# Kernel optimization log

Hardware: AMD Instinct MI355X
Metric: run time of the kernel (lower is better)

## Reference

```python
import jax, jax.numpy as jnp
import numpy as np

EPS = 1e-05

def setup_inputs() -> dict:
    key = jax.random.key(0)
    k1, = jax.random.split(key, 1)
    x = jax.random.normal(k1, (4, 4096, 2048), dtype=jnp.float32)
    g = jnp.ones((2048,), dtype=jnp.float32)
    return {"x": x, "g": g}

def reference(x, g):
    # RMSNorm: x / sqrt(mean(x^2, axis=-1) + eps) * g, computed in fp32
    dtype = x.dtype
    xf = x.astype(jnp.float32)
    ms = jnp.mean(xf * xf, axis=-1, keepdims=True)  # [B,S,1]
    out = xf * jax.lax.rsqrt(ms + EPS) * g
    return out.astype(dtype)
```

## Files before the change

### kernel.cpp

```cpp
#include <hip/hip_runtime.h>

#define ROW_LEN 2048
#define BLOCK   256
#define ROWS_PER_BLOCK 4
#define EPS     1e-5f

__global__ __launch_bounds__(BLOCK) void RMSNorm_56607668961691_kernel(
    const float* __restrict__ x,
    const float* __restrict__ g,
    float* __restrict__ out)
{
    const int wave = threadIdx.x >> 6;
    const int lane = threadIdx.x & 63;
    const size_t row = (size_t)blockIdx.x * ROWS_PER_BLOCK + wave;

    const float4* __restrict__ xr   = reinterpret_cast<const float4*>(x + row * ROW_LEN) + lane;
    float4* __restrict__       outr = reinterpret_cast<float4*>(out + row * ROW_LEN) + lane;
    const float4* __restrict__ gv   = reinterpret_cast<const float4*>(g) + lane;

    float4 v[8];
    #pragma unroll
    for (int j = 0; j < 8; ++j) v[j] = xr[j * 64];

    float s0 = 0.f, s1 = 0.f, s2 = 0.f, s3 = 0.f;
    #pragma unroll
    for (int j = 0; j < 8; ++j) {
        s0 += v[j].x * v[j].x;
        s1 += v[j].y * v[j].y;
        s2 += v[j].z * v[j].z;
        s3 += v[j].w * v[j].w;
    }
    float ss = (s0 + s1) + (s2 + s3);

    #pragma unroll
    for (int off = 32; off > 0; off >>= 1)
        ss += __shfl_xor(ss, off, 64);

    const float scale = rsqrtf(ss * (1.0f / (float)ROW_LEN) + EPS);

    #pragma unroll
    for (int j = 0; j < 8; ++j) {
        const float4 gj = gv[j * 64];
        float4 o;
        o.x = v[j].x * scale * gj.x;
        o.y = v[j].y * scale * gj.y;
        o.z = v[j].z * scale * gj.z;
        o.w = v[j].w * scale * gj.w;
        outr[j * 64] = o;
    }
}

extern "C" void kernel_launch(void* const* d_in, const int* in_sizes, int n_in,
                              void* d_out, int out_size, void* d_ws, size_t ws_size,
                              hipStream_t stream) {
    const float* x = (const float*)d_in[0];
    const float* g = (const float*)d_in[1];
    float* out = (float*)d_out;

    const int rows = in_sizes[0] / ROW_LEN;
    const int grid = rows / ROWS_PER_BLOCK;
    RMSNorm_56607668961691_kernel<<<grid, BLOCK, 0, stream>>>(x, g, out);
}
```

Baseline: 229.3 us.

## Process four rows per wave with register prefetch and nontemporal stores

Each wave now handles four consecutive rows. It loads the gamma vector once and prefetches the next row into registers while the current row is reduced and written. Output writes use nontemporal stores to avoid polluting the cache, and the grid shrinks by four. In exchange, register pressure rises and the grid has far fewer blocks, which may reduce the memory-level parallelism the GPU can use to hide latency.

```diff
diff --git a/kernel.cpp b/kernel.cpp
--- a/kernel.cpp
+++ b/kernel.cpp
@@ -2,51 +2,74 @@
 
 #define ROW_LEN 2048
 #define BLOCK   256
-#define ROWS_PER_BLOCK 4
+#define ROWS_PER_WAVE 4
 #define EPS     1e-5f
 
-__global__ __launch_bounds__(BLOCK) void RMSNorm_56607668961691_kernel(
+typedef float floatx4 __attribute__((ext_vector_type(4)));
+
+__global__ __launch_bounds__(BLOCK, 4) void RMSNorm_56607668961691_kernel(
     const float* __restrict__ x,
     const float* __restrict__ g,
     float* __restrict__ out)
 {
     const int wave = threadIdx.x >> 6;
     const int lane = threadIdx.x & 63;
-    const size_t row = (size_t)blockIdx.x * ROWS_PER_BLOCK + wave;
+    const size_t wid  = (size_t)blockIdx.x * (BLOCK / 64) + wave;
+    const size_t row0 = wid * ROWS_PER_WAVE;
 
-    const float4* __restrict__ xr   = reinterpret_cast<const float4*>(x + row * ROW_LEN) + lane;
-    float4* __restrict__       outr = reinterpret_cast<float4*>(out + row * ROW_LEN) + lane;
+    const float4* __restrict__ xr   = reinterpret_cast<const float4*>(x + row0 * ROW_LEN) + lane;
+    float4* __restrict__       outr = reinterpret_cast<float4*>(out + row0 * ROW_LEN) + lane;
     const float4* __restrict__ gv   = reinterpret_cast<const float4*>(g) + lane;
 
-    float4 v[8];
+    float4 gr[8];
     #pragma unroll
-    for (int j = 0; j < 8; ++j) v[j] = xr[j * 64];
+    for (int j = 0; j < 8; ++j) gr[j] = gv[j * 64];
 
-    float s0 = 0.f, s1 = 0.f, s2 = 0.f, s3 = 0.f;
+    float4 cur[8];
     #pragma unroll
-    for (int j = 0; j < 8; ++j) {
-        s0 += v[j].x * v[j].x;
-        s1 += v[j].y * v[j].y;
-        s2 += v[j].z * v[j].z;
-        s3 += v[j].w * v[j].w;
-    }
-    float ss = (s0 + s1) + (s2 + s3);
+    for (int j = 0; j < 8; ++j) cur[j] = xr[j * 64];
 
     #pragma unroll
-    for (int off = 32; off > 0; off >>= 1)
-        ss += __shfl_xor(ss, off, 64);
+    for (int r = 0; r < ROWS_PER_WAVE; ++r) {
+        float4 nxt[8];
+        if (r + 1 < ROWS_PER_WAVE) {
+            const float4* xn = xr + (size_t)(r + 1) * (ROW_LEN / 4);
+            #pragma unroll
+            for (int j = 0; j < 8; ++j) nxt[j] = xn[j * 64];
+        }
 
-    const float scale = rsqrtf(ss * (1.0f / (float)ROW_LEN) + EPS);
+        float s0 = 0.f, s1 = 0.f, s2 = 0.f, s3 = 0.f;
+        #pragma unroll
+        for (int j = 0; j < 8; ++j) {
+            s0 += cur[j].x * cur[j].x;
+            s1 += cur[j].y * cur[j].y;
+            s2 += cur[j].z * cur[j].z;
+            s3 += cur[j].w * cur[j].w;
+        }
+        float ss = (s0 + s1) + (s2 + s3);
 
-    #pragma unroll
-    for (int j = 0; j < 8; ++j) {
-        const float4 gj = gv[j * 64];
-        float4 o;
-        o.x = v[j].x * scale * gj.x;
-        o.y = v[j].y * scale * gj.y;
-        o.z = v[j].z * scale * gj.z;
-        o.w = v[j].w * scale * gj.w;
-        outr[j * 64] = o;
+        #pragma unroll
+        for (int off = 32; off > 0; off >>= 1)
+            ss += __shfl_xor(ss, off, 64);
+
+        const float scale = rsqrtf(ss * (1.0f / (float)ROW_LEN) + EPS);
+
+        float4* o = outr + (size_t)r * (ROW_LEN / 4);
+        #pragma unroll
+        for (int j = 0; j < 8; ++j) {
+            float4 ov;
+            ov.x = cur[j].x * scale * gr[j].x;
+            ov.y = cur[j].y * scale * gr[j].y;
+            ov.z = cur[j].z * scale * gr[j].z;
+            ov.w = cur[j].w * scale * gr[j].w;
+            __builtin_nontemporal_store(*reinterpret_cast<floatx4*>(&ov),
+                                        reinterpret_cast<floatx4*>(&o[j * 64]));
+        }
+
+        if (r + 1 < ROWS_PER_WAVE) {
+            #pragma unroll
+            for (int j = 0; j < 8; ++j) cur[j] = nxt[j];
+        }
     }
 }
 
@@ -58,6 +81,6 @@
     float* out = (float*)d_out;
 
     const int rows = in_sizes[0] / ROW_LEN;
-    const int grid = rows / ROWS_PER_BLOCK;
+    const int grid = rows / (ROWS_PER_WAVE * (BLOCK / 64));
     RMSNorm_56607668961691_kernel<<<grid, BLOCK, 0, stream>>>(x, g, out);
 }
```

Result: slower. 234.8 us (+2.4%).

## Split RMSNorm into row-scale pass and streaming elementwise pass

Applied to the files above, without the earlier changes.

Computes per-row inverse RMS in a first kernel into a global scale buffer, then applies scale and gain in a second grid-stride streaming kernel with nontemporal stores. The intent is to decouple the reduction from a fully coalesced, high-occupancy elementwise pass. It costs a second full read of x and an extra launch, and relies on a fixed-size global scale array.

```diff
diff --git a/kernel.cpp b/kernel.cpp
--- a/kernel.cpp
+++ b/kernel.cpp
@@ -2,21 +2,22 @@
 
 #define ROW_LEN 2048
 #define BLOCK   256
-#define ROWS_PER_BLOCK 4
 #define EPS     1e-5f
 
-__global__ __launch_bounds__(BLOCK) void RMSNorm_56607668961691_kernel(
-    const float* __restrict__ x,
-    const float* __restrict__ g,
-    float* __restrict__ out)
+typedef float floatx4 __attribute__((ext_vector_type(4)));
+
+__device__ float g_row_scale[32768];
+
+__global__ __launch_bounds__(BLOCK) void RMSNorm_pass1_kernel(
+    const float* __restrict__ x, int rows)
 {
     const int wave = threadIdx.x >> 6;
     const int lane = threadIdx.x & 63;
-    const size_t row = (size_t)blockIdx.x * ROWS_PER_BLOCK + wave;
+    const int row  = blockIdx.x * (BLOCK / 64) + wave;
+    if (row >= rows) return;
 
-    const float4* __restrict__ xr   = reinterpret_cast<const float4*>(x + row * ROW_LEN) + lane;
-    float4* __restrict__       outr = reinterpret_cast<float4*>(out + row * ROW_LEN) + lane;
-    const float4* __restrict__ gv   = reinterpret_cast<const float4*>(g) + lane;
+    const float4* __restrict__ xr =
+        reinterpret_cast<const float4*>(x + (size_t)row * ROW_LEN) + lane;
 
     float4 v[8];
     #pragma unroll
@@ -36,17 +37,27 @@
     for (int off = 32; off > 0; off >>= 1)
         ss += __shfl_xor(ss, off, 64);
 
-    const float scale = rsqrtf(ss * (1.0f / (float)ROW_LEN) + EPS);
+    if (lane == 0)
+        g_row_scale[row] = rsqrtf(ss * (1.0f / (float)ROW_LEN) + EPS);
+}
 
-    #pragma unroll
-    for (int j = 0; j < 8; ++j) {
-        const float4 gj = gv[j * 64];
-        float4 o;
-        o.x = v[j].x * scale * gj.x;
-        o.y = v[j].y * scale * gj.y;
-        o.z = v[j].z * scale * gj.z;
-        o.w = v[j].w * scale * gj.w;
-        outr[j * 64] = o;
+__global__ __launch_bounds__(BLOCK) void RMSNorm_pass2_kernel(
+    const float* __restrict__ x, const float* __restrict__ g,
+    float* __restrict__ out, int n4)
+{
+    const floatx4* __restrict__ x4 = reinterpret_cast<const floatx4*>(x);
+    const floatx4* __restrict__ g4 = reinterpret_cast<const floatx4*>(g);
+    floatx4* __restrict__       o4 = reinterpret_cast<floatx4*>(out);
+
+    const int stride = gridDim.x * BLOCK;
+    for (int i = blockIdx.x * BLOCK + threadIdx.x; i < n4; i += stride) {
+        const floatx4 xv = x4[i];
+        const int row = i >> 9;
+        const int col = i & 511;
+        const float s = g_row_scale[row];
+        const floatx4 gv = g4[col];
+        floatx4 ov = xv * s * gv;
+        __builtin_nontemporal_store(ov, &o4[i]);
     }
 }
 
@@ -58,6 +69,11 @@
     float* out = (float*)d_out;
 
     const int rows = in_sizes[0] / ROW_LEN;
-    const int grid = rows / ROWS_PER_BLOCK;
-    RMSNorm_56607668961691_kernel<<<grid, BLOCK, 0, stream>>>(x, g, out);
+    const int n4   = rows * (ROW_LEN / 4);
+
+    const int grid1 = (rows + (BLOCK / 64) - 1) / (BLOCK / 64);
+    RMSNorm_pass1_kernel<<<grid1, BLOCK, 0, stream>>>(x, rows);
+
+    const int grid2 = 4096;
+    RMSNorm_pass2_kernel<<<grid2, BLOCK, 0, stream>>>(x, g, out, n4);
 }
```

After: 245.9 us. +7.3%, slower.

## Split block into producer/consumer waves with double-buffered LDS row pipeline

Applied to the files above, without the earlier changes.

Restructures the kernel so that four producer waves load a row into LDS and compute partial sums of squares, while four consumer waves normalize and store the previous row. Each block now handles 8 rows in sequence, with block-wide barriers between steps. The goal is to overlap global loads with stores through a software pipeline. In exchange it adds LDS round trips, a __syncthreads per row, and fewer independent outstanding loads per thread, on a kernel that is purely memory-bound.

```diff
diff --git a/kernel.cpp b/kernel.cpp
--- a/kernel.cpp
+++ b/kernel.cpp
@@ -1,8 +1,9 @@
 #include <hip/hip_runtime.h>
 
 #define ROW_LEN 2048
-#define BLOCK   256
-#define ROWS_PER_BLOCK 4
+#define R4      (ROW_LEN / 4)
+#define BLOCK   512
+#define ROWS_PER_BLOCK 8
 #define EPS     1e-5f
 
 __global__ __launch_bounds__(BLOCK) void RMSNorm_56607668961691_kernel(
@@ -10,43 +11,58 @@
     const float* __restrict__ g,
     float* __restrict__ out)
 {
-    const int wave = threadIdx.x >> 6;
-    const int lane = threadIdx.x & 63;
-    const size_t row = (size_t)blockIdx.x * ROWS_PER_BLOCK + wave;
+    __shared__ float4 buf[2][R4];
+    __shared__ float  psum[2][4];
 
-    const float4* __restrict__ xr   = reinterpret_cast<const float4*>(x + row * ROW_LEN) + lane;
-    float4* __restrict__       outr = reinterpret_cast<float4*>(out + row * ROW_LEN) + lane;
-    const float4* __restrict__ gv   = reinterpret_cast<const float4*>(g) + lane;
+    const int tid  = threadIdx.x;
+    const int w    = tid >> 6;
+    const int lane = tid & 63;
+    const bool producer = (w < 4);
+    const int pw   = producer ? w : (w - 4);
+    const int c    = pw * 64 + lane;
 
-    float4 v[8];
-    #pragma unroll
-    for (int j = 0; j < 8; ++j) v[j] = xr[j * 64];
+    const size_t row0 = (size_t)blockIdx.x * ROWS_PER_BLOCK;
+    const float4* __restrict__ x4 = reinterpret_cast<const float4*>(x) + row0 * R4;
+    float4* __restrict__       o4 = reinterpret_cast<float4*>(out)     + row0 * R4;
+    const float4* __restrict__ g4 = reinterpret_cast<const float4*>(g);
 
-    float s0 = 0.f, s1 = 0.f, s2 = 0.f, s3 = 0.f;
-    #pragma unroll
-    for (int j = 0; j < 8; ++j) {
-        s0 += v[j].x * v[j].x;
-        s1 += v[j].y * v[j].y;
-        s2 += v[j].z * v[j].z;
-        s3 += v[j].w * v[j].w;
-    }
-    float ss = (s0 + s1) + (s2 + s3);
+    float4 ga, gb;
+    if (!producer) { ga = g4[c]; gb = g4[c + 256]; }
 
-    #pragma unroll
-    for (int off = 32; off > 0; off >>= 1)
-        ss += __shfl_xor(ss, off, 64);
-
-    const float scale = rsqrtf(ss * (1.0f / (float)ROW_LEN) + EPS);
-
-    #pragma unroll
-    for (int j = 0; j < 8; ++j) {
-        const float4 gj = gv[j * 64];
-        float4 o;
-        o.x = v[j].x * scale * gj.x;
-        o.y = v[j].y * scale * gj.y;
-        o.z = v[j].z * scale * gj.z;
-        o.w = v[j].w * scale * gj.w;
-        outr[j * 64] = o;
+    for (int t = 0; t <= ROWS_PER_BLOCK; ++t) {
+        const int b = t & 1;
+        if (producer) {
+            if (t < ROWS_PER_BLOCK) {
+                const float4 v0 = x4[(size_t)t * R4 + c];
+                const float4 v1 = x4[(size_t)t * R4 + c + 256];
+                buf[b][c]       = v0;
+                buf[b][c + 256] = v1;
+                float s = v0.x * v0.x + v0.y * v0.y + v0.z * v0.z + v0.w * v0.w
+                        + v1.x * v1.x + v1.y * v1.y + v1.z * v1.z + v1.w * v1.w;
+                #pragma unroll
+                for (int off = 32; off > 0; off >>= 1)
+                    s += __shfl_xor(s, off, 64);
+                if (lane == 0) psum[b][pw] = s;
+            }
+        } else {
+            if (t > 0) {
+                const int bb = b ^ 1;
+                const int tr = t - 1;
+                const float total = psum[bb][0] + psum[bb][1]
+                                  + psum[bb][2] + psum[bb][3];
+                const float scale = rsqrtf(total * (1.0f / (float)ROW_LEN) + EPS);
+                const float4 v0 = buf[bb][c];
+                const float4 v1 = buf[bb][c + 256];
+                float4 o0, o1;
+                o0.x = v0.x * scale * ga.x;  o0.y = v0.y * scale * ga.y;
+                o0.z = v0.z * scale * ga.z;  o0.w = v0.w * scale * ga.w;
+                o1.x = v1.x * scale * gb.x;  o1.y = v1.y * scale * gb.y;
+                o1.z = v1.z * scale * gb.z;  o1.w = v1.w * scale * gb.w;
+                o4[(size_t)tr * R4 + c]       = o0;
+                o4[(size_t)tr * R4 + c + 256] = o1;
+            }
+        }
+        __syncthreads();
     }
 }
 
```

After: 236.2 us. 3.0% more time.
